# Kernel tuning notes

Hardware: AMD Instinct MI355X
Metric: run time of the kernel (lower is better)

Reference implementation:

```python
import jax, jax.numpy as jnp
from jax import lax
import numpy as np

B, T, F, H, NC = 64, 4096, 40, 128, 12


def setup_inputs() -> dict:
    key = jax.random.key(0)
    ks = jax.random.split(key, 20)
    s = 0.05
    inp = {
        "x": jax.random.normal(ks[0], (B, 1, T, F), dtype=jnp.float32),
        # LSTM layer 0 (PyTorch layout: W_ih [4H, in], W_hh [4H, H], gate order i,f,g,o)
        "W_ih0": jax.random.normal(ks[1], (4 * H, F), dtype=jnp.float32) * s,
        "W_hh0": jax.random.normal(ks[2], (4 * H, H), dtype=jnp.float32) * s,
        "b_ih0": jax.random.normal(ks[3], (4 * H,), dtype=jnp.float32) * s,
        "b_hh0": jax.random.normal(ks[4], (4 * H,), dtype=jnp.float32) * s,
        # LSTM layer 1
        "W_ih1": jax.random.normal(ks[5], (4 * H, H), dtype=jnp.float32) * s,
        "W_hh1": jax.random.normal(ks[6], (4 * H, H), dtype=jnp.float32) * s,
        "b_ih1": jax.random.normal(ks[7], (4 * H,), dtype=jnp.float32) * s,
        "b_hh1": jax.random.normal(ks[8], (4 * H,), dtype=jnp.float32) * s,
        # attention params
        "weight_W": jax.random.normal(ks[9], (H, H), dtype=jnp.float32) * s,
        "bias": jax.random.normal(ks[10], (H, 1), dtype=jnp.float32) * s,
        "weight_proj": jax.random.normal(ks[11], (H, 1), dtype=jnp.float32) * s,
        # classifier head
        "dnn1_w": jax.random.normal(ks[12], (64, H), dtype=jnp.float32) * s,
        "dnn1_b": jax.random.normal(ks[13], (64,), dtype=jnp.float32) * s,
        "out_w": jax.random.normal(ks[14], (NC, 64), dtype=jnp.float32) * s,
        "out_b": jax.random.normal(ks[15], (NC,), dtype=jnp.float32) * s,
    }
    return inp


def _lstm_layer(inp, W_ih, W_hh, b_ih, b_hh):
    # inp: [T, B, in_dim]; returns hidden states [T, B, H]
    Hh = W_hh.shape[1]
    Bb = inp.shape[1]

    def step(carry, x_t):
        h, c = carry
        g = x_t @ W_ih.T + b_ih + h @ W_hh.T + b_hh  # [B, 4H]
        i, f, gg, o = jnp.split(g, 4, axis=-1)
        c = jax.nn.sigmoid(f) * c + jax.nn.sigmoid(i) * jnp.tanh(gg)
        h = jax.nn.sigmoid(o) * jnp.tanh(c)
        return (h, c), h

    init = (jnp.zeros((Bb, Hh), inp.dtype), jnp.zeros((Bb, Hh), inp.dtype))
    _, hs = lax.scan(step, init, inp)
    return hs


def reference(x, W_ih0, W_hh0, b_ih0, b_hh0, W_ih1, W_hh1, b_ih1, b_hh1,
              weight_W, bias, weight_proj, dnn1_w, dnn1_b, out_w, out_b):
    # [B,1,T,F] -> [T,B,F]
    xs = x.reshape(x.shape[0], x.shape[2], x.shape[3]).transpose(1, 0, 2)
    h = _lstm_layer(xs, W_ih0, W_hh0, b_ih0, b_hh0)   # [T,B,H] (dropout eval = identity)
    h = _lstm_layer(h, W_ih1, W_hh1, b_ih1, b_hh1)    # [T,B,H]
    # batch_matmul_bias with tanh, fully batched: tanh(h @ W + b)
    squish = jnp.tanh(jnp.einsum('tbh,hk->tbk', h, weight_W) + bias[:, 0])  # [T,B,H]
    # batch_matmul with proj -> scores [T,B]
    attn = jnp.einsum('tbh,ho->tb', squish, weight_proj)
    # softmax over time (dim=1 after transpose to [B,T] == axis 0 here)
    attn_norm = jax.nn.softmax(attn, axis=0)          # [T,B]
    # attention_mul: weighted sum over time
    ctx = jnp.einsum('tb,tbh->bh', attn_norm, h)      # [B,H]
    y = ctx @ dnn1_w.T + dnn1_b                       # dropout eval = identity
    return y @ out_w.T + out_b                        # [B, NC]
```

## Files before the change

kernel.cpp:

```cpp
#include <hip/hip_runtime.h>
#include <cstddef>

#define TT 4096
#define BB 64
#define HD 128
#define G4 512
#define FD 40
#define NCLS 12
#define CH 256
#define NCHUNK 16

typedef float v2f __attribute__((ext_vector_type(2)));

__device__ __forceinline__ float sigf(float x){ return 1.0f/(1.0f + __expf(-x)); }
__device__ __forceinline__ float tanh_f(float x){ return 1.0f - 2.0f/(__expf(2.0f*x) + 1.0f); }

__global__ void whh_pack(const float* __restrict__ W, float* __restrict__ WPf){
  int idx = blockIdx.x*256 + threadIdx.x;
  int k2 = idx >> 9;
  int j  = idx & 511;
  float2 v = make_float2(W[j*HD + 2*k2], W[j*HD + 2*k2 + 1]);
  ((float2*)WPf)[idx] = v;
}

__global__ __launch_bounds__(512, 2)
void lstm_rec_dual(const float* __restrict__ preA, const float* __restrict__ wpA,
                   float* __restrict__ houtA, float* __restrict__ stateA,
                   const float* __restrict__ preB, const float* __restrict__ wpB,
                   float* __restrict__ houtB, float* __restrict__ stateB,
                   int nsteps)
{
  int bb = blockIdx.x;
  const float* pre; const float* wpf; float* hout; float* state;
  if (bb < 64){ pre = preA; wpf = wpA; hout = houtA; state = stateA; }
  else        { pre = preB; wpf = wpB; hout = houtB; state = stateB; bb -= 64; }

  const int t = threadIdx.x;
  __shared__ __align__(16) float h_lds[HD];
  __shared__ float g_lds[G4];

  const v2f* wp = (const v2f*)wpf;
  v2f w[64];
#pragma unroll
  for (int j=0;j<64;j++) w[j] = wp[j*512 + t];

  float c = 0.0f;
  if (t < HD){
    h_lds[t] = state[bb*256 + t];
    c = state[bb*256 + 128 + t];
  }
  __syncthreads();

  const float* prep = pre + (size_t)bb*G4 + t;
  float pg = prep[0];

  for (int s=0; s<nsteps; ++s){
    int sn = (s+1 < nsteps) ? (s+1) : s;
    float npg = prep[(size_t)sn*(BB*G4)];

    v2f acc0; acc0.x = pg; acc0.y = 0.0f;
    v2f acc1; acc1.x = 0.0f; acc1.y = 0.0f;
#pragma unroll
    for (int j=0;j<64;j+=2){
      float4 h4 = *(const float4*)&h_lds[j*2];
      v2f h01; h01.x = h4.x; h01.y = h4.y;
      v2f h23; h23.x = h4.z; h23.y = h4.w;
      acc0 = __builtin_elementwise_fma(w[j],   h01, acc0);
      acc1 = __builtin_elementwise_fma(w[j+1], h23, acc1);
    }
    float g = (acc0.x + acc1.x) + (acc0.y + acc1.y);

    g_lds[t] = g;
    asm volatile("s_waitcnt lgkmcnt(0)" ::: "memory");
    __builtin_amdgcn_s_barrier();
    __builtin_amdgcn_sched_barrier(0);

    if (t < HD){
      float gi = g;
      float gf = g_lds[t + 128];
      float gg = g_lds[t + 256];
      float go = g_lds[t + 384];
      c = sigf(gf)*c + sigf(gi)*tanh_f(gg);
      float h = sigf(go)*tanh_f(c);
      h_lds[t] = h;
      hout[((size_t)s*BB + bb)*HD + t] = h;
    }
    asm volatile("s_waitcnt lgkmcnt(0)" ::: "memory");
    __builtin_amdgcn_s_barrier();
    __builtin_amdgcn_sched_barrier(0);

    pg = npg;
  }

  if (t < HD){
    state[bb*256 + t] = h_lds[t];
    state[bb*256 + 128 + t] = c;
  }
}

template<int AMODE, int BTRANS, int KD, int EPI>
__global__ __launch_bounds__(256)
void gemm_k(const float* __restrict__ A, const float* __restrict__ Bw,
            const float* __restrict__ b1, const float* __restrict__ b2,
            float* __restrict__ C, int t0)
{
  const int tid = threadIdx.x;
  const int tx = tid & 15, ty = tid >> 4;
  const int m0 = blockIdx.x * 128;
  const int n0 = blockIdx.y * 128;
  const int NDIM = EPI ? 128 : 512;
  __shared__ __align__(16) float Ast[8*128];
  __shared__ __align__(16) float Bst[8*128];
  __shared__ float red[128*17];
  float acc[8][8];
#pragma unroll
  for (int i=0;i<8;i++)
#pragma unroll
    for (int j=0;j<8;j++) acc[i][j]=0.f;

  const int NK = KD/8;
  for (int kt=0; kt<NK; ++kt){
    const int k0 = kt*8;
    const int arow = tid >> 1;
    const int akq = (tid & 1) * 4;
    const float* aptr;
    if (AMODE == 0){
      aptr = A + (size_t)(m0 + arow)*KD + k0 + akq;
    } else {
      int m = m0 + arow;
      int bidx = m & 63;
      int trow = t0 + (m >> 6);
      aptr = A + ((size_t)bidx*TT + trow)*FD + k0 + akq;
    }
    float4 av = *(const float4*)aptr;
    float4 bv;
    int brow, bkq;
    if (BTRANS){
      brow = tid >> 1; bkq = (tid & 1) * 4;
      bv = *(const float4*)(Bw + (size_t)(n0 + brow)*KD + k0 + bkq);
    } else {
      brow = tid >> 5;
      bkq = (tid & 31) * 4;
      bv = *(const float4*)(Bw + (size_t)(k0 + brow)*NDIM + n0 + bkq);
    }
    __syncthreads();
    Ast[(akq+0)*128 + arow] = av.x;
    Ast[(akq+1)*128 + arow] = av.y;
    Ast[(akq+2)*128 + arow] = av.z;
    Ast[(akq+3)*128 + arow] = av.w;
    if (BTRANS){
      Bst[(bkq+0)*128 + brow] = bv.x;
      Bst[(bkq+1)*128 + brow] = bv.y;
      Bst[(bkq+2)*128 + brow] = bv.z;
      Bst[(bkq+3)*128 + brow] = bv.w;
    } else {
      *(float4*)&Bst[brow*128 + bkq] = bv;
    }
    __syncthreads();
#pragma unroll
    for (int kk=0; kk<8; ++kk){
      float a[8], bbv[8];
      *(float4*)&a[0]   = *(const float4*)&Ast[kk*128 + ty*8];
      *(float4*)&a[4]   = *(const float4*)&Ast[kk*128 + ty*8 + 4];
      *(float4*)&bbv[0] = *(const float4*)&Bst[kk*128 + tx*8];
      *(float4*)&bbv[4] = *(const float4*)&Bst[kk*128 + tx*8 + 4];
#pragma unroll
      for (int i=0;i<8;i++)
#pragma unroll
        for (int j=0;j<8;j++) acc[i][j] = fmaf(a[i], bbv[j], acc[i][j]);
    }
  }
  if (EPI == 0){
    const int nb = n0 + tx*8;
    float bias[8];
#pragma unroll
    for (int j=0;j<8;j++) bias[j] = b1[nb+j] + b2[nb+j];
#pragma unroll
    for (int i=0;i<8;i++){
      int m = m0 + ty*8 + i;
      float* cp = C + (size_t)m*NDIM + nb;
      float4 o0 = make_float4(acc[i][0]+bias[0], acc[i][1]+bias[1], acc[i][2]+bias[2], acc[i][3]+bias[3]);
      float4 o1 = make_float4(acc[i][4]+bias[4], acc[i][5]+bias[5], acc[i][6]+bias[6], acc[i][7]+bias[7]);
      *(float4*)&cp[0] = o0;
      *(float4*)&cp[4] = o1;
    }
  } else {
    const int nb = tx*8;
    float bias[8], proj[8];
#pragma unroll
    for (int j=0;j<8;j++){ bias[j] = b1[nb+j]; proj[j] = b2[nb+j]; }
#pragma unroll
    for (int i=0;i<8;i++){
      float p = 0.f;
#pragma unroll
      for (int j=0;j<8;j++) p += tanh_f(acc[i][j] + bias[j]) * proj[j];
      red[(ty*8+i)*17 + tx] = p;
    }
    __syncthreads();
    if (tid < 128){
      float s = 0.f;
#pragma unroll
      for (int xx=0; xx<16; ++xx) s += red[tid*17 + xx];
      C[m0 + tid] = s;
    }
  }
}

__global__ void softmax_t(float* __restrict__ attn){
  const int b = blockIdx.x;
  const int tid = threadIdx.x;
  __shared__ float red[256];
  float v[16];
  float m = -1e30f;
#pragma unroll
  for (int i=0;i<16;i++){
    v[i] = attn[(i*256 + tid)*BB + b];
    m = fmaxf(m, v[i]);
  }
  red[tid] = m; __syncthreads();
  for (int s=128; s>0; s>>=1){ if (tid < s) red[tid] = fmaxf(red[tid], red[tid+s]); __syncthreads(); }
  m = red[0]; __syncthreads();
  float sum = 0.f;
#pragma unroll
  for (int i=0;i<16;i++){ v[i] = __expf(v[i]-m); sum += v[i]; }
  red[tid] = sum; __syncthreads();
  for (int s=128; s>0; s>>=1){ if (tid < s) red[tid] += red[tid+s]; __syncthreads(); }
  float inv = 1.0f/red[0];
#pragma unroll
  for (int i=0;i<16;i++) attn[(i*256 + tid)*BB + b] = v[i]*inv;
}

__global__ void ctx_k(const float* __restrict__ attn, const float* __restrict__ h1,
                      float* __restrict__ ctxp){
  const int b = blockIdx.x;
  const int g = blockIdx.y;
  const int h = threadIdx.x;
  float acc = 0.f;
  const int tb = g*512;
#pragma unroll 4
  for (int i=0;i<512;i++){
    int t = tb + i;
    acc = fmaf(attn[t*BB + b], h1[((size_t)t*BB + b)*HD + h], acc);
  }
  ctxp[((size_t)b*8 + g)*HD + h] = acc;
}

__global__ void head_k(const float* __restrict__ ctxp, const float* __restrict__ d1w,
                       const float* __restrict__ d1b, const float* __restrict__ ow,
                       const float* __restrict__ ob, float* __restrict__ out){
  const int b = blockIdx.x;
  const int tid = threadIdx.x;
  __shared__ float cl[128];
  __shared__ float yl[64];
  for (int i=tid; i<128; i+=64){
    float s = 0.f;
#pragma unroll
    for (int g=0; g<8; g++) s += ctxp[((size_t)b*8 + g)*HD + i];
    cl[i] = s;
  }
  __syncthreads();
  float y = d1b[tid];
#pragma unroll 8
  for (int k=0;k<128;k++) y = fmaf(cl[k], d1w[tid*128 + k], y);
  yl[tid] = y;
  __syncthreads();
  if (tid < NCLS){
    float o = ob[tid];
#pragma unroll 8
    for (int j=0;j<64;j++) o = fmaf(yl[j], ow[tid*64 + j], o);
    out[b*NCLS + tid] = o;
  }
}

extern "C" void kernel_launch(void* const* d_in, const int* in_sizes, int n_in,
                              void* d_out, int out_size, void* d_ws, size_t ws_size,
                              hipStream_t stream) {
  const float* x     = (const float*)d_in[0];
  const float* Wih0  = (const float*)d_in[1];
  const float* Whh0  = (const float*)d_in[2];
  const float* bih0  = (const float*)d_in[3];
  const float* bhh0  = (const float*)d_in[4];
  const float* Wih1  = (const float*)d_in[5];
  const float* Whh1  = (const float*)d_in[6];
  const float* bih1  = (const float*)d_in[7];
  const float* bhh1  = (const float*)d_in[8];
  const float* wW    = (const float*)d_in[9];
  const float* bias  = (const float*)d_in[10];
  const float* proj  = (const float*)d_in[11];
  const float* d1w   = (const float*)d_in[12];
  const float* d1b   = (const float*)d_in[13];
  const float* ow    = (const float*)d_in[14];
  const float* ob    = (const float*)d_in[15];

  float* ws = (float*)d_ws;
  float* state0 = ws;
  float* state1 = state0 + 16384;
  float* WP0    = state1 + 16384;
  float* WP1    = WP0 + 65536;
  float* pre0   = WP1 + 65536;
  float* pre1   = pre0 + (size_t)CH*BB*G4;
  float* h0c    = pre1 + (size_t)CH*BB*G4;
  float* h1     = h0c + (size_t)CH*BB*HD;
  float* attn   = h1 + (size_t)TT*BB*HD;
  float* ctxp   = attn + (size_t)TT*BB;

  hipMemsetAsync(state0, 0, 2*16384*sizeof(float), stream);
  whh_pack<<<128, 256, 0, stream>>>(Whh0, WP0);
  whh_pack<<<128, 256, 0, stream>>>(Whh1, WP1);

  gemm_k<1,1,40,0><<<dim3(CH*BB/128, 4), 256, 0, stream>>>(x, Wih0, bih0, bhh0, pre0, 0);
  lstm_rec_dual<<<64, 512, 0, stream>>>(pre0, WP0, h0c, state0,
                                        pre0, WP0, h0c, state0, CH);
  for (int k=1; k<NCHUNK; ++k){
    int t0A = (k-1)*CH;
    int t0B = k*CH;
    gemm_k<0,1,128,0><<<dim3(CH*BB/128, 4), 256, 0, stream>>>(h0c, Wih1, bih1, bhh1, pre1, 0);
    gemm_k<1,1,40,0><<<dim3(CH*BB/128, 4), 256, 0, stream>>>(x, Wih0, bih0, bhh0, pre0, t0B);
    lstm_rec_dual<<<128, 512, 0, stream>>>(pre1, WP1, h1 + (size_t)t0A*BB*HD, state1,
                                           pre0, WP0, h0c, state0, CH);
  }
  gemm_k<0,1,128,0><<<dim3(CH*BB/128, 4), 256, 0, stream>>>(h0c, Wih1, bih1, bhh1, pre1, 0);
  lstm_rec_dual<<<64, 512, 0, stream>>>(pre1, WP1, h1 + (size_t)(NCHUNK-1)*CH*BB*HD, state1,
                                        pre1, WP1, h1 + (size_t)(NCHUNK-1)*CH*BB*HD, state1, CH);

  gemm_k<0,0,128,1><<<dim3(TT*BB/128, 1), 256, 0, stream>>>(h1, wW, bias, proj, attn, 0);
  softmax_t<<<64, 256, 0, stream>>>(attn);
  ctx_k<<<dim3(64, 8), 128, 0, stream>>>(attn, h1, ctxp);
  head_k<<<64, 64, 0, stream>>>(ctxp, d1w, d1b, ow, ob, (float*)d_out);
}
```

Before: 4.746 ms.

## Pair LSTM gates per thread pair to remove gate LDS exchange and barrier

The recurrent LSTM kernel now uses 256 threads per batch row instead of 512. Each thread computes two gate rows, and a thread pair jointly holds all four gates (i,f,g,o) for one hidden unit. Gates are exchanged with a lane shuffle instead of shared memory, and the hidden state is double-buffered in LDS, so each step needs one barrier instead of two. This removes the g_lds round trip and one block-wide sync per time step. In exchange each thread holds 128 register float2 weights, which raises register pressure and halves the threads per block.

```diff
diff --git a/kernel.cpp b/kernel.cpp
--- a/kernel.cpp
+++ b/kernel.cpp
@@ -15,20 +15,24 @@
 __device__ __forceinline__ float sigf(float x){ return 1.0f/(1.0f + __expf(-x)); }
 __device__ __forceinline__ float tanh_f(float x){ return 1.0f - 2.0f/(__expf(2.0f*x) + 1.0f); }
 
-__global__ void whh_pack(const float* __restrict__ W, float* __restrict__ WPf){
+__global__ void whh_pack2(const float* __restrict__ W, float* __restrict__ WPf){
   int idx = blockIdx.x*256 + threadIdx.x;
-  int k2 = idx >> 9;
-  int j  = idx & 511;
-  float2 v = make_float2(W[j*HD + 2*k2], W[j*HD + 2*k2 + 1]);
-  ((float2*)WPf)[idx] = v;
-}
-
-__global__ __launch_bounds__(512, 2)
-void lstm_rec_dual(const float* __restrict__ preA, const float* __restrict__ wpA,
-                   float* __restrict__ houtA, float* __restrict__ stateA,
-                   const float* __restrict__ preB, const float* __restrict__ wpB,
-                   float* __restrict__ houtB, float* __restrict__ stateB,
-                   int nsteps)
+  int which = idx >> 14;
+  int rem = idx & 16383;
+  int k2 = rem >> 8;
+  int t  = rem & 255;
+  int j = t >> 1, odd = t & 1;
+  int rA = (odd ? 128 : 0) + j;
+  int row = which ? (rA + 256) : rA;
+  ((float2*)WPf)[idx] = make_float2(W[row*HD + 2*k2], W[row*HD + 2*k2 + 1]);
+}
+
+__global__ __launch_bounds__(256, 1)
+void lstm_rec3(const float* __restrict__ preA, const float* __restrict__ wpA,
+               float* __restrict__ houtA, float* __restrict__ stateA,
+               const float* __restrict__ preB, const float* __restrict__ wpB,
+               float* __restrict__ houtB, float* __restrict__ stateB,
+               int nsteps)
 {
   int bb = blockIdx.x;
   const float* pre; const float* wpf; float* hout; float* state;
@@ -36,65 +40,76 @@
   else        { pre = preB; wpf = wpB; hout = houtB; state = stateB; bb -= 64; }
 
   const int t = threadIdx.x;
-  __shared__ __align__(16) float h_lds[HD];
-  __shared__ float g_lds[G4];
+  const int j = t >> 1;
+  const int odd = t & 1;
+
+  __shared__ __align__(16) float h_lds[2][HD];
 
   const v2f* wp = (const v2f*)wpf;
-  v2f w[64];
-#pragma unroll
-  for (int j=0;j<64;j++) w[j] = wp[j*512 + t];
-
-  float c = 0.0f;
-  if (t < HD){
-    h_lds[t] = state[bb*256 + t];
-    c = state[bb*256 + 128 + t];
-  }
+  v2f wA[64], wB[64];
+#pragma unroll
+  for (int k2=0;k2<64;k2++) wA[k2] = wp[k2*256 + t];
+#pragma unroll
+  for (int k2=0;k2<64;k2++) wB[k2] = wp[16384 + k2*256 + t];
+
+  float c = state[bb*256 + 128 + j];
+  if (t < HD) h_lds[0][t] = state[bb*256 + t];
   __syncthreads();
 
-  const float* prep = pre + (size_t)bb*G4 + t;
-  float pg = prep[0];
-
+  const int rA = (odd ? 128 : 0) + j;
+  const float* prepA = pre + (size_t)bb*G4 + rA;
+  const float* prepB = prepA + 256;
+  float pgA = prepA[0];
+  float pgB = prepB[0];
+
+  int cur = 0;
+  float h = 0.0f;
   for (int s=0; s<nsteps; ++s){
     int sn = (s+1 < nsteps) ? (s+1) : s;
-    float npg = prep[(size_t)sn*(BB*G4)];
-
-    v2f acc0; acc0.x = pg; acc0.y = 0.0f;
-    v2f acc1; acc1.x = 0.0f; acc1.y = 0.0f;
-#pragma unroll
-    for (int j=0;j<64;j+=2){
-      float4 h4 = *(const float4*)&h_lds[j*2];
+    float npgA = prepA[(size_t)sn*(BB*G4)];
+    float npgB = prepB[(size_t)sn*(BB*G4)];
+
+    v2f a0; a0.x = pgA; a0.y = 0.0f;
+    v2f a1; a1.x = pgB; a1.y = 0.0f;
+#pragma unroll
+    for (int k4=0;k4<32;k4++){
+      float4 h4 = *(const float4*)&h_lds[cur][k4*4];
       v2f h01; h01.x = h4.x; h01.y = h4.y;
       v2f h23; h23.x = h4.z; h23.y = h4.w;
-      acc0 = __builtin_elementwise_fma(w[j],   h01, acc0);
-      acc1 = __builtin_elementwise_fma(w[j+1], h23, acc1);
-    }
-    float g = (acc0.x + acc1.x) + (acc0.y + acc1.y);
-
-    g_lds[t] = g;
+      a0 = __builtin_elementwise_fma(wA[2*k4],   h01, a0);
+      a1 = __builtin_elementwise_fma(wB[2*k4],   h01, a1);
+      a0 = __builtin_elementwise_fma(wA[2*k4+1], h23, a0);
+      a1 = __builtin_elementwise_fma(wB[2*k4+1], h23, a1);
+    }
+    float gA = a0.x + a0.y;
+    float gB = a1.x + a1.y;
+
+    float oA = __shfl_xor(gA, 1, 64);
+    float oB = __shfl_xor(gB, 1, 64);
+    float gi = odd ? oA : gA;
+    float gf = odd ? gA : oA;
+    float gg = odd ? oB : gB;
+    float go = odd ? gB : oB;
+
+    c = sigf(gf)*c + sigf(gi)*tanh_f(gg);
+    h = sigf(go)*tanh_f(c);
+
+    int nxt = cur ^ 1;
+    if (!odd){
+      h_lds[nxt][j] = h;
+      hout[((size_t)s*BB + bb)*HD + j] = h;
+    }
     asm volatile("s_waitcnt lgkmcnt(0)" ::: "memory");
     __builtin_amdgcn_s_barrier();
     __builtin_amdgcn_sched_barrier(0);
 
-    if (t < HD){
-      float gi = g;
-      float gf = g_lds[t + 128];
-      float gg = g_lds[t + 256];
-      float go = g_lds[t + 384];
-      c = sigf(gf)*c + sigf(gi)*tanh_f(gg);
-      float h = sigf(go)*tanh_f(c);
-      h_lds[t] = h;
-      hout[((size_t)s*BB + bb)*HD + t] = h;
-    }
-    asm volatile("s_waitcnt lgkmcnt(0)" ::: "memory");
-    __builtin_amdgcn_s_barrier();
-    __builtin_amdgcn_sched_barrier(0);
-
-    pg = npg;
-  }
-
-  if (t < HD){
-    state[bb*256 + t] = h_lds[t];
-    state[bb*256 + 128 + t] = c;
+    cur = nxt;
+    pgA = npgA; pgB = npgB;
+  }
+
+  if (!odd){
+    state[bb*256 + j] = h;
+    state[bb*256 + 128 + j] = c;
   }
 }
 
@@ -305,23 +320,23 @@
   float* ctxp   = attn + (size_t)TT*BB;
 
   hipMemsetAsync(state0, 0, 2*16384*sizeof(float), stream);
-  whh_pack<<<128, 256, 0, stream>>>(Whh0, WP0);
-  whh_pack<<<128, 256, 0, stream>>>(Whh1, WP1);
+  whh_pack2<<<128, 256, 0, stream>>>(Whh0, WP0);
+  whh_pack2<<<128, 256, 0, stream>>>(Whh1, WP1);
 
   gemm_k<1,1,40,0><<<dim3(CH*BB/128, 4), 256, 0, stream>>>(x, Wih0, bih0, bhh0, pre0, 0);
-  lstm_rec_dual<<<64, 512, 0, stream>>>(pre0, WP0, h0c, state0,
-                                        pre0, WP0, h0c, state0, CH);
+  lstm_rec3<<<64, 256, 0, stream>>>(pre0, WP0, h0c, state0,
+                                    pre0, WP0, h0c, state0, CH);
   for (int k=1; k<NCHUNK; ++k){
     int t0A = (k-1)*CH;
     int t0B = k*CH;
     gemm_k<0,1,128,0><<<dim3(CH*BB/128, 4), 256, 0, stream>>>(h0c, Wih1, bih1, bhh1, pre1, 0);
     gemm_k<1,1,40,0><<<dim3(CH*BB/128, 4), 256, 0, stream>>>(x, Wih0, bih0, bhh0, pre0, t0B);
-    lstm_rec_dual<<<128, 512, 0, stream>>>(pre1, WP1, h1 + (size_t)t0A*BB*HD, state1,
-                                           pre0, WP0, h0c, state0, CH);
+    lstm_rec3<<<128, 256, 0, stream>>>(pre1, WP1, h1 + (size_t)t0A*BB*HD, state1,
+                                       pre0, WP0, h0c, state0, CH);
   }
   gemm_k<0,1,128,0><<<dim3(CH*BB/128, 4), 256, 0, stream>>>(h0c, Wih1, bih1, bhh1, pre1, 0);
-  lstm_rec_dual<<<64, 512, 0, stream>>>(pre1, WP1, h1 + (size_t)(NCHUNK-1)*CH*BB*HD, state1,
-                                        pre1, WP1, h1 + (size_t)(NCHUNK-1)*CH*BB*HD, state1, CH);
+  lstm_rec3<<<64, 256, 0, stream>>>(pre1, WP1, h1 + (size_t)(NCHUNK-1)*CH*BB*HD, state1,
+                                    pre1, WP1, h1 + (size_t)(NCHUNK-1)*CH*BB*HD, state1, CH);
 
   gemm_k<0,0,128,1><<<dim3(TT*BB/128, 1), 256, 0, stream>>>(h1, wW, bias, proj, attn, 0);
   softmax_t<<<64, 256, 0, stream>>>(attn);
```

Result: slower. 7.632 ms (+60.8%).
